# Optimization experiments

Measured on AMD Instinct MI355X. Metric: run time of the kernel, lower is better.

Reference implementation:

```python
import jax, jax.numpy as jnp
import numpy as np

N_NODES = 50000
N_EDGES = 1200000
D_FEAT = 64
HIDDEN = 32


def setup_inputs() -> dict:
    key = jax.random.key(0)
    ks = jax.random.split(key, 9)
    x = jax.random.normal(ks[0], (N_NODES, D_FEAT), dtype=jnp.float32)
    edge_index = jax.random.randint(ks[1], (2, N_EDGES), 0, N_NODES, dtype=jnp.int64)
    u = jax.random.normal(ks[2], (N_NODES,), dtype=jnp.float32)
    d_in = 2 * D_FEAT
    # MLP: Linear(d_in,H) -> relu -> Linear(H,H) -> relu -> Linear(H,1)
    W1 = jax.random.normal(ks[3], (d_in, HIDDEN), dtype=jnp.float32) / np.sqrt(d_in)
    b1 = jnp.zeros((HIDDEN,), dtype=jnp.float32)
    W2 = jax.random.normal(ks[4], (HIDDEN, HIDDEN), dtype=jnp.float32) / np.sqrt(HIDDEN)
    b2 = jnp.zeros((HIDDEN,), dtype=jnp.float32)
    W3 = jax.random.normal(ks[5], (HIDDEN, 1), dtype=jnp.float32) / np.sqrt(HIDDEN)
    b3 = jnp.zeros((1,), dtype=jnp.float32)
    return {"x": x, "edge_index": edge_index, "u": u,
            "W1": W1, "b1": b1, "W2": W2, "b2": b2, "W3": W3, "b3": b3}


def reference(x, edge_index, u, W1, b1, W2, b2, W3, b3):
    row, col = edge_index[0], edge_index[1]
    # gather + concat: [E, 2*D]
    x_edge = jnp.concatenate([x[row], x[col]], axis=-1)
    # per-edge MLP -> scalar weight per edge
    h = jax.nn.relu(x_edge @ W1 + b1)
    h = jax.nn.relu(h @ W2 + b2)
    edge_weight = (h @ W3 + b3)[:, 0]  # [E]
    # spmm: f[i] = sum_{e: row[e]==i} w_e * u[col[e]]
    f = jax.ops.segment_sum(edge_weight * u[col], row, num_segments=x.shape[0])
    return f
```

## Files before the change

### kernel.cpp

```cpp
#include <hip/hip_runtime.h>
#include <hip/hip_bf16.h>

#define N_NODES 50000
#define N_EDGES 1200000
#define N_TILES (N_NODES / 16)
#define W1T_STRIDE 72
#define K1_BLOCKS 782

#define N_BUCKETS 196
#define BUCKET_CAP 7168
#define EDGES_PER_BLOCK 1920
#define KA_BLOCKS 625
#define D1_BLOCKS (K1_BLOCKS + KA_BLOCKS)
#define KB_SPLIT 4

typedef __attribute__((ext_vector_type(8))) short short8;
typedef __attribute__((ext_vector_type(4))) float floatx4;

__device__ __forceinline__ unsigned short f32_to_bf16(float f) {
    unsigned int v = __float_as_uint(f);
    unsigned int r = v + 0x7FFFu + ((v >> 16) & 1u);
    return (unsigned short)(r >> 16);
}
__device__ __forceinline__ float bf16_to_f32(unsigned short s) {
    return __uint_as_float(((unsigned int)s) << 16);
}
__device__ __forceinline__ unsigned int pk_bf16x2_rn(float lo, float hi) {
    union { __hip_bfloat162 h; unsigned int u; } cv;
    cv.h = __float22bfloat162_rn(make_float2(lo, hi));
    return cv.u;
}
#define DPP_ROR_F32(x, N) \
    __int_as_float(__builtin_amdgcn_update_dpp( \
        0, __float_as_int(x), 0x120 + (N), 0xF, 0xF, false))

__global__ __launch_bounds__(256) void fused_pre_bin(
    const float* __restrict__ x, const float* __restrict__ W1,
    const float* __restrict__ b1,
    const int* __restrict__ row, const int* __restrict__ col,
    unsigned short* __restrict__ P1, unsigned short* __restrict__ P2,
    unsigned int* __restrict__ buf, int* __restrict__ cursor,
    float* __restrict__ out)
{
    __shared__ union {
        unsigned short W1t[64 * W1T_STRIDE];
        struct {
            unsigned short rankv[EDGES_PER_BLOCK];
            int hist[N_BUCKETS];
            int base[N_BUCKETS];
        } bin;
    } sh;

    const int tid = threadIdx.x;
    const int bid = blockIdx.x;

    if (bid < K1_BLOCKS) {
        const int gtid = bid * 256 + tid;
        for (int i = gtid; i < N_NODES; i += K1_BLOCKS * 256)
            out[i] = 0.0f;

        for (int e = tid; e < 128 * 32; e += 256) {
            const int kp = e >> 5, jp = e & 31;
            sh.W1t[((kp < 64) ? jp : jp + 32) * W1T_STRIDE + (kp & 63)] =
                f32_to_bf16(W1[e]);
        }
        __syncthreads();

        const int lane = tid & 63;
        const int n = lane & 15;
        const int q = lane >> 4;

        const int tile = bid * 4 + (tid >> 6);
        if (tile >= N_TILES) return;

        short8 bw[4][2];
        #pragma unroll
        for (int G = 0; G < 4; ++G)
            #pragma unroll
            for (int h = 0; h < 2; ++h)
                bw[G][h] = *(const short8*)
                    &sh.W1t[(n + 16 * G) * W1T_STRIDE + h * 32 + q * 8];
        const float bias0 = b1[n], bias1 = b1[n + 16];

        const int node = tile * 16 + n;
        const float4* xp  = (const float4*)(x + (size_t)node * 64 + q * 8);
        const float4 xa = xp[0], xb = xp[1];
        const float4* xp2 = (const float4*)(x + (size_t)node * 64 + 32 + q * 8);
        const float4 xc = xp2[0], xd = xp2[1];

        union S8 { short8 s; unsigned int w[4]; } A0, A1;
        A0.w[0] = pk_bf16x2_rn(xa.x, xa.y);
        A0.w[1] = pk_bf16x2_rn(xa.z, xa.w);
        A0.w[2] = pk_bf16x2_rn(xb.x, xb.y);
        A0.w[3] = pk_bf16x2_rn(xb.z, xb.w);
        A1.w[0] = pk_bf16x2_rn(xc.x, xc.y);
        A1.w[1] = pk_bf16x2_rn(xc.z, xc.w);
        A1.w[2] = pk_bf16x2_rn(xd.x, xd.y);
        A1.w[3] = pk_bf16x2_rn(xd.z, xd.w);
        const short8 a0 = A0.s, a1 = A1.s;

        floatx4 acc[4];
        #pragma unroll
        for (int G = 0; G < 4; ++G) {
            const float bi = (G == 0) ? bias0 : (G == 1) ? bias1 : 0.0f;
            acc[G] = (floatx4){bi, bi, bi, bi};
            acc[G] = __builtin_amdgcn_mfma_f32_16x16x32_bf16(a0, bw[G][0], acc[G], 0, 0, 0);
            acc[G] = __builtin_amdgcn_mfma_f32_16x16x32_bf16(a1, bw[G][1], acc[G], 0, 0, 0);
        }
        unsigned int* P1d = (unsigned int*)P1;
        unsigned int* P2d = (unsigned int*)P2;
        #pragma unroll
        for (int r = 0; r < 4; ++r) {
            const int nr = tile * 16 + q * 4 + r;
            P1d[(size_t)nr * 16 + n] = pk_bf16x2_rn(acc[0][r], acc[1][r]);
            P2d[(size_t)nr * 16 + n] = pk_bf16x2_rn(acc[2][r], acc[3][r]);
        }
    } else {
        for (int b = tid; b < N_BUCKETS; b += 256) sh.bin.hist[b] = 0;
        __syncthreads();

        const int blockStart = (bid - K1_BLOCKS) * EDGES_PER_BLOCK;

        for (int i = tid; i < EDGES_PER_BLOCK; i += 256) {
            const int r = row[blockStart + i];
            sh.bin.rankv[i] = (unsigned short)atomicAdd(&sh.bin.hist[r >> 8], 1);
        }
        __syncthreads();

        for (int b = tid; b < N_BUCKETS; b += 256)
            sh.bin.base[b] = atomicAdd(&cursor[b], sh.bin.hist[b]);
        __syncthreads();

        for (int i = tid; i < EDGES_PER_BLOCK; i += 256) {
            const int r = row[blockStart + i];
            const int c = col[blockStart + i];
            const int bin = r >> 8;
            buf[(size_t)bin * BUCKET_CAP + sh.bin.base[bin] + (int)sh.bin.rankv[i]] =
                ((unsigned int)(r & 255) << 24) | (unsigned int)c;
        }
    }
}

__global__ __launch_bounds__(512) void bucket_mlp(
    const float* __restrict__ u,
    const float* __restrict__ W2, const float* __restrict__ b2,
    const float* __restrict__ W3, const float* __restrict__ b3,
    const unsigned short* __restrict__ P1, const unsigned short* __restrict__ P2,
    const unsigned int* __restrict__ buf, const int* __restrict__ cursor,
    float* __restrict__ out)
{
    __shared__ float accs[256];
    const int tid = threadIdx.x;
    if (tid < 256) accs[tid] = 0.0f;

    const int b = blockIdx.x >> 2;
    const int s = blockIdx.x & (KB_SPLIT - 1);

    const int lane = tid & 63;
    const int n = lane & 15;
    const int q = lane >> 4;
    const int wave = tid >> 6;

    short8 bf0, bf1;
    #pragma unroll
    for (int i = 0; i < 8; ++i) {
        const int F = q * 4 + (i >> 1) + 16 * (i & 1);
        bf0[i] = (short)f32_to_bf16(W2[F * 32 + n]);
        bf1[i] = (short)f32_to_bf16(W2[F * 32 + n + 16]);
    }
    const float w3n0 = W3[n], w3n1 = W3[n + 16];
    const float b2n0 = b2[n], b2n1 = b2[n + 16];
    const float bias3 = b3[0];

    __syncthreads();

    const int cnt = cursor[b];
    const unsigned int* bb = buf + (size_t)b * BUCKET_CAP;
    const unsigned short* P1b = P1 + (size_t)b * 256 * 32;
    const int nch = (cnt + 31) >> 5;

    #pragma unroll 1
    for (int ch = s * 8 + wave; ch < nch; ch += KB_SPLIT * 8) {
        const int base0 = ch * 32;

        int rl[2], cI[2];
        #pragma unroll
        for (int t = 0; t < 2; ++t) {
            int e = base0 + t * 16 + n;
            if (e >= cnt) e = cnt - 1;
            const unsigned int ent = bb[e];
            rl[t] = (int)(ent >> 24);
            cI[t] = (int)(ent & 0x1FFFFu);
        }
        int r2 = 0; float u2 = 0.0f;
        if (n < 8) {
            const int eloc = base0 + 16 * (n >> 2) + 4 * q + (n & 3);
            const unsigned int ent2 = bb[(eloc < cnt) ? eloc : 0];
            r2 = (int)(ent2 >> 24);
            u2 = (eloc < cnt) ? u[ent2 & 0x1FFFFu] : 0.0f;
        }
        short8 v1[2], v2[2];
        #pragma unroll
        for (int t = 0; t < 2; ++t) {
            v1[t] = *(const short8*)(P1b + (size_t)rl[t] * 32 + q * 8);
            v2[t] = *(const short8*)(P2 + (size_t)cI[t] * 32 + q * 8);
        }

        float tr[2][4];
        #pragma unroll
        for (int t = 0; t < 2; ++t) {
            union VU { short8 s; unsigned int w[4]; };
            VU x1, x2, ar;
            x1.s = v1[t]; x2.s = v2[t];
            #pragma unroll
            for (int i = 0; i < 4; ++i) {
                const unsigned int w1 = x1.w[i], w2 = x2.w[i];
                float lo = __uint_as_float(w1 << 16) + __uint_as_float(w2 << 16);
                float hi = __uint_as_float(w1 & 0xFFFF0000u)
                         + __uint_as_float(w2 & 0xFFFF0000u);
                lo = fmaxf(lo, 0.0f);
                hi = fmaxf(hi, 0.0f);
                ar.w[i] = pk_bf16x2_rn(lo, hi);
            }
            const short8 a = ar.s;
            floatx4 d0 = {b2n0, b2n0, b2n0, b2n0};
            floatx4 d1 = {b2n1, b2n1, b2n1, b2n1};
            d0 = __builtin_amdgcn_mfma_f32_16x16x32_bf16(a, bf0, d0, 0, 0, 0);
            d1 = __builtin_amdgcn_mfma_f32_16x16x32_bf16(a, bf1, d1, 0, 0, 0);
            #pragma unroll
            for (int r = 0; r < 4; ++r)
                tr[t][r] = fmaxf(d0[r], 0.0f) * w3n0 + fmaxf(d1[r], 0.0f) * w3n1;
        }

        #pragma unroll
        for (int t = 0; t < 2; ++t)
            #pragma unroll
            for (int r = 0; r < 4; ++r) {
                float v = tr[t][r];
                v += DPP_ROR_F32(v, 1);
                v += DPP_ROR_F32(v, 2);
                v += DPP_ROR_F32(v, 4);
                v += DPP_ROR_F32(v, 8);
                tr[t][r] = v;
            }

        if (n < 8) {
            const float va0 = (n & 4) ? tr[1][0] : tr[0][0];
            const float va1 = (n & 4) ? tr[1][1] : tr[0][1];
            const float va2 = (n & 4) ? tr[1][2] : tr[0][2];
            const float va3 = (n & 4) ? tr[1][3] : tr[0][3];
            const float vb0 = (n & 2) ? va2 : va0;
            const float vb1 = (n & 2) ? va3 : va1;
            const float v   = (n & 1) ? vb1 : vb0;
            atomicAdd(&accs[r2], (v + bias3) * u2);
        }
    }

    __syncthreads();

    if (tid < 256) {
        const int node = b * 256 + tid;
        if (node < N_NODES) atomicAdd(out + node, accs[tid]);
    }
}

extern "C" void kernel_launch(void* const* d_in, const int* in_sizes, int n_in,
                              void* d_out, int out_size, void* d_ws, size_t ws_size,
                              hipStream_t stream)
{
    const float* x    = (const float*)d_in[0];
    const int*   eidx = (const int*)  d_in[1];
    const float* u    = (const float*)d_in[2];
    const float* W1   = (const float*)d_in[3];
    const float* b1   = (const float*)d_in[4];
    const float* W2   = (const float*)d_in[5];
    const float* b2   = (const float*)d_in[6];
    const float* W3   = (const float*)d_in[7];
    const float* b3   = (const float*)d_in[8];

    const int* row = eidx;
    const int* col = eidx + N_EDGES;

    unsigned short* P1 = (unsigned short*)d_ws;
    unsigned short* P2 = (unsigned short*)((char*)d_ws + (size_t)N_NODES * 64);
    unsigned int*  buf = (unsigned int*)((char*)d_ws + (size_t)N_NODES * 128);
    int* cursor = (int*)((char*)d_ws + (size_t)N_NODES * 128
                         + (size_t)N_BUCKETS * BUCKET_CAP * 4);
    float* out = (float*)d_out;

    hipMemsetAsync(cursor, 0, N_BUCKETS * sizeof(int), stream);

    fused_pre_bin<<<D1_BLOCKS, 256, 0, stream>>>(
        x, W1, b1, row, col, P1, P2, buf, cursor, out);

    bucket_mlp<<<N_BUCKETS * KB_SPLIT, 512, 0, stream>>>(
        u, W2, b2, W3, b3, P1, P2, buf, cursor, out);
}
```

Before: 132.1 us.

## Merge memset, prebin and bucket MLP into one cooperative persistent kernel

Replaces the memset plus two kernel launches with a single cooperative kernel that uses grid-wide syncs between zeroing, the binning/first-layer GEMM phase, and the per-bucket MLP/scatter phase. Work is distributed as persistent tasks over a grid sized from occupancy, and the bucket phase now uses 256-thread blocks with 8 splits per bucket instead of 512-thread blocks with 4. The aim is to remove launch gaps and the memset, at the cost of grid.sync overhead and a different occupancy/work balance. The old path is kept as a fallback when the cooperative launch fails.

```diff
diff --git a/kernel.cpp b/kernel.cpp
--- a/kernel.cpp
+++ b/kernel.cpp
@@ -1,18 +1,27 @@
 #include <hip/hip_runtime.h>
 #include <hip/hip_bf16.h>
+#include <hip/hip_cooperative_groups.h>
+
+namespace cg = cooperative_groups;
 
 #define N_NODES 50000
 #define N_EDGES 1200000
 #define N_TILES (N_NODES / 16)
-#define W1T_STRIDE 72
-#define K1_BLOCKS 782
 
 #define N_BUCKETS 196
 #define BUCKET_CAP 7168
 #define EDGES_PER_BLOCK 1920
 #define KA_BLOCKS 625
+#define GEMM_BLOCKS 782
+#define A1_TASKS (KA_BLOCKS + GEMM_BLOCKS)
+#define KB_SPLIT8 8
+#define KB_TASKS (N_BUCKETS * KB_SPLIT8)
+#define MAX_COOP_GRID 2048
+
+#define W1T_STRIDE_FB 72
+#define K1_BLOCKS 782
 #define D1_BLOCKS (K1_BLOCKS + KA_BLOCKS)
-#define KB_SPLIT 4
+#define KB_SPLIT_FB 4
 
 typedef __attribute__((ext_vector_type(8))) short short8;
 typedef __attribute__((ext_vector_type(4))) float floatx4;
@@ -33,6 +42,237 @@
 #define DPP_ROR_F32(x, N) \
     __int_as_float(__builtin_amdgcn_update_dpp( \
         0, __float_as_int(x), 0x120 + (N), 0xF, 0xF, false))
+
+__global__ __launch_bounds__(256, 8) void edgemlp_coop(
+    const float* __restrict__ x, const float* __restrict__ W1,
+    const float* __restrict__ b1,
+    const int* __restrict__ row, const int* __restrict__ col,
+    const float* __restrict__ u,
+    const float* __restrict__ W2, const float* __restrict__ b2,
+    const float* __restrict__ W3, const float* __restrict__ b3,
+    unsigned short* __restrict__ P1, unsigned short* __restrict__ P2,
+    unsigned int* __restrict__ buf, int* __restrict__ cursor,
+    float* __restrict__ out)
+{
+    __shared__ union {
+        unsigned short W1t[64 * 64];
+        struct {
+            unsigned short rankv[EDGES_PER_BLOCK];
+            int hist[N_BUCKETS];
+            int base[N_BUCKETS];
+        } bin;
+        float accs[256];
+    } sh;
+
+    cg::grid_group grid = cg::this_grid();
+
+    const int tid = threadIdx.x;
+    const int bid = blockIdx.x;
+    const int gstride = (int)gridDim.x;
+    const int gtid = bid * 256 + tid;
+
+    const int lane = tid & 63;
+    const int n = lane & 15;
+    const int q = lane >> 4;
+    const int wave = tid >> 6;
+
+    for (int i = gtid; i < N_NODES; i += gstride * 256) out[i] = 0.0f;
+    if (gtid < N_BUCKETS) cursor[gtid] = 0;
+
+    grid.sync();
+
+    for (int task = bid; task < A1_TASKS; task += gstride) {
+        if (task < KA_BLOCKS) {
+            for (int b = tid; b < N_BUCKETS; b += 256) sh.bin.hist[b] = 0;
+            __syncthreads();
+
+            const int blockStart = task * EDGES_PER_BLOCK;
+
+            for (int i = tid; i < EDGES_PER_BLOCK; i += 256) {
+                const int r = row[blockStart + i];
+                sh.bin.rankv[i] =
+                    (unsigned short)atomicAdd(&sh.bin.hist[r >> 8], 1);
+            }
+            __syncthreads();
+
+            for (int b = tid; b < N_BUCKETS; b += 256)
+                sh.bin.base[b] = atomicAdd(&cursor[b], sh.bin.hist[b]);
+            __syncthreads();
+
+            for (int i = tid; i < EDGES_PER_BLOCK; i += 256) {
+                const int r = row[blockStart + i];
+                const int c = col[blockStart + i];
+                const int bin = r >> 8;
+                buf[(size_t)bin * BUCKET_CAP + sh.bin.base[bin]
+                    + (int)sh.bin.rankv[i]] =
+                    ((unsigned int)(r & 255) << 24) | (unsigned int)c;
+            }
+        } else {
+            for (int e = tid; e < 128 * 32; e += 256) {
+                const int kp = e >> 5, jp = e & 31;
+                sh.W1t[((kp < 64) ? jp : jp + 32) * 64 + (kp & 63)] =
+                    f32_to_bf16(W1[e]);
+            }
+            __syncthreads();
+
+            const int tile = (task - KA_BLOCKS) * 4 + wave;
+            if (tile < N_TILES) {
+                short8 bw[4][2];
+                #pragma unroll
+                for (int G = 0; G < 4; ++G)
+                    #pragma unroll
+                    for (int h = 0; h < 2; ++h)
+                        bw[G][h] = *(const short8*)
+                            &sh.W1t[(n + 16 * G) * 64 + h * 32 + q * 8];
+                const float bias0 = b1[n], bias1 = b1[n + 16];
+
+                const int node = tile * 16 + n;
+                const float4* xp  = (const float4*)(x + (size_t)node * 64 + q * 8);
+                const float4 xa = xp[0], xb = xp[1];
+                const float4* xp2 = (const float4*)(x + (size_t)node * 64 + 32 + q * 8);
+                const float4 xc = xp2[0], xd = xp2[1];
+
+                union S8 { short8 s; unsigned int w[4]; } A0v, A1v;
+                A0v.w[0] = pk_bf16x2_rn(xa.x, xa.y);
+                A0v.w[1] = pk_bf16x2_rn(xa.z, xa.w);
+                A0v.w[2] = pk_bf16x2_rn(xb.x, xb.y);
+                A0v.w[3] = pk_bf16x2_rn(xb.z, xb.w);
+                A1v.w[0] = pk_bf16x2_rn(xc.x, xc.y);
+                A1v.w[1] = pk_bf16x2_rn(xc.z, xc.w);
+                A1v.w[2] = pk_bf16x2_rn(xd.x, xd.y);
+                A1v.w[3] = pk_bf16x2_rn(xd.z, xd.w);
+                const short8 a0 = A0v.s, a1 = A1v.s;
+
+                floatx4 acc[4];
+                #pragma unroll
+                for (int G = 0; G < 4; ++G) {
+                    const float bi = (G == 0) ? bias0 : (G == 1) ? bias1 : 0.0f;
+                    acc[G] = (floatx4){bi, bi, bi, bi};
+                    acc[G] = __builtin_amdgcn_mfma_f32_16x16x32_bf16(a0, bw[G][0], acc[G], 0, 0, 0);
+                    acc[G] = __builtin_amdgcn_mfma_f32_16x16x32_bf16(a1, bw[G][1], acc[G], 0, 0, 0);
+                }
+                unsigned int* P1d = (unsigned int*)P1;
+                unsigned int* P2d = (unsigned int*)P2;
+                #pragma unroll
+                for (int r = 0; r < 4; ++r) {
+                    const int nr = tile * 16 + q * 4 + r;
+                    P1d[(size_t)nr * 16 + n] = pk_bf16x2_rn(acc[0][r], acc[1][r]);
+                    P2d[(size_t)nr * 16 + n] = pk_bf16x2_rn(acc[2][r], acc[3][r]);
+                }
+            }
+        }
+        __syncthreads();
+    }
+
+    grid.sync();
+
+    short8 bf0, bf1;
+    #pragma unroll
+    for (int i = 0; i < 8; ++i) {
+        const int F = q * 4 + (i >> 1) + 16 * (i & 1);
+        bf0[i] = (short)f32_to_bf16(W2[F * 32 + n]);
+        bf1[i] = (short)f32_to_bf16(W2[F * 32 + n + 16]);
+    }
+    const float w3n0 = W3[n], w3n1 = W3[n + 16];
+    const float b2n0 = b2[n], b2n1 = b2[n + 16];
+    const float bias3 = b3[0];
+
+    for (int task = bid; task < KB_TASKS; task += gstride) {
+        const int b = task >> 3;
+        const int s = task & (KB_SPLIT8 - 1);
+
+        sh.accs[tid] = 0.0f;
+        __syncthreads();
+
+        const int cnt = cursor[b];
+        const unsigned int* bb = buf + (size_t)b * BUCKET_CAP;
+        const unsigned short* P1b = P1 + (size_t)b * 256 * 32;
+        const int nch = (cnt + 31) >> 5;
+
+        #pragma unroll 1
+        for (int ch = s * 4 + wave; ch < nch; ch += 32) {
+            const int base0 = ch * 32;
+
+            int rl[2], cI[2];
+            #pragma unroll
+            for (int t = 0; t < 2; ++t) {
+                int e = base0 + t * 16 + n;
+                if (e >= cnt) e = cnt - 1;
+                const unsigned int ent = bb[e];
+                rl[t] = (int)(ent >> 24);
+                cI[t] = (int)(ent & 0x1FFFFu);
+            }
+            int r2 = 0; float u2 = 0.0f;
+            if (n < 8) {
+                const int eloc = base0 + 16 * (n >> 2) + 4 * q + (n & 3);
+                const unsigned int ent2 = bb[(eloc < cnt) ? eloc : 0];
+                r2 = (int)(ent2 >> 24);
+                u2 = (eloc < cnt) ? u[ent2 & 0x1FFFFu] : 0.0f;
+            }
+            short8 v1[2], v2[2];
+            #pragma unroll
+            for (int t = 0; t < 2; ++t) {
+                v1[t] = *(const short8*)(P1b + (size_t)rl[t] * 32 + q * 8);
+                v2[t] = *(const short8*)(P2 + (size_t)cI[t] * 32 + q * 8);
+            }
+
+            float tr[2][4];
+            #pragma unroll
+            for (int t = 0; t < 2; ++t) {
+                union VU { short8 s; unsigned int w[4]; };
+                VU x1, x2, ar;
+                x1.s = v1[t]; x2.s = v2[t];
+                #pragma unroll
+                for (int i = 0; i < 4; ++i) {
+                    const unsigned int w1 = x1.w[i], w2 = x2.w[i];
+                    float lo = __uint_as_float(w1 << 16) + __uint_as_float(w2 << 16);
+                    float hi = __uint_as_float(w1 & 0xFFFF0000u)
+                             + __uint_as_float(w2 & 0xFFFF0000u);
+                    lo = fmaxf(lo, 0.0f);
+                    hi = fmaxf(hi, 0.0f);
+                    ar.w[i] = pk_bf16x2_rn(lo, hi);
+                }
+                const short8 a = ar.s;
+                floatx4 d0 = {b2n0, b2n0, b2n0, b2n0};
+                floatx4 d1 = {b2n1, b2n1, b2n1, b2n1};
+                d0 = __builtin_amdgcn_mfma_f32_16x16x32_bf16(a, bf0, d0, 0, 0, 0);
+                d1 = __builtin_amdgcn_mfma_f32_16x16x32_bf16(a, bf1, d1, 0, 0, 0);
+                #pragma unroll
+                for (int r = 0; r < 4; ++r)
+                    tr[t][r] = fmaxf(d0[r], 0.0f) * w3n0 + fmaxf(d1[r], 0.0f) * w3n1;
+            }
+
+            #pragma unroll
+            for (int t = 0; t < 2; ++t)
+                #pragma unroll
+                for (int r = 0; r < 4; ++r) {
+                    float v = tr[t][r];
+                    v += DPP_ROR_F32(v, 1);
+                    v += DPP_ROR_F32(v, 2);
+                    v += DPP_ROR_F32(v, 4);
+                    v += DPP_ROR_F32(v, 8);
+                    tr[t][r] = v;
+                }
+
+            if (n < 8) {
+                const float va0 = (n & 4) ? tr[1][0] : tr[0][0];
+                const float va1 = (n & 4) ? tr[1][1] : tr[0][1];
+                const float va2 = (n & 4) ? tr[1][2] : tr[0][2];
+                const float va3 = (n & 4) ? tr[1][3] : tr[0][3];
+                const float vb0 = (n & 2) ? va2 : va0;
+                const float vb1 = (n & 2) ? va3 : va1;
+                const float v   = (n & 1) ? vb1 : vb0;
+                atomicAdd(&sh.accs[r2], (v + bias3) * u2);
+            }
+        }
+
+        __syncthreads();
+
+        const int node = b * 256 + tid;
+        if (node < N_NODES) atomicAdd(out + node, sh.accs[tid]);
+        __syncthreads();
+    }
+}
 
 __global__ __launch_bounds__(256) void fused_pre_bin(
     const float* __restrict__ x, const float* __restrict__ W1,
@@ -43,7 +283,7 @@
     float* __restrict__ out)
 {
     __shared__ union {
-        unsigned short W1t[64 * W1T_STRIDE];
+        unsigned short W1t[64 * W1T_STRIDE_FB];
         struct {
             unsigned short rankv[EDGES_PER_BLOCK];
             int hist[N_BUCKETS];
@@ -61,7 +301,7 @@
 
         for (int e = tid; e < 128 * 32; e += 256) {
             const int kp = e >> 5, jp = e & 31;
-            sh.W1t[((kp < 64) ? jp : jp + 32) * W1T_STRIDE + (kp & 63)] =
+            sh.W1t[((kp < 64) ? jp : jp + 32) * W1T_STRIDE_FB + (kp & 63)] =
                 f32_to_bf16(W1[e]);
         }
         __syncthreads();
@@ -79,7 +319,7 @@
             #pragma unroll
             for (int h = 0; h < 2; ++h)
                 bw[G][h] = *(const short8*)
-                    &sh.W1t[(n + 16 * G) * W1T_STRIDE + h * 32 + q * 8];
+                    &sh.W1t[(n + 16 * G) * W1T_STRIDE_FB + h * 32 + q * 8];
         const float bias0 = b1[n], bias1 = b1[n + 16];
 
         const int node = tile * 16 + n;
@@ -154,7 +394,7 @@
     if (tid < 256) accs[tid] = 0.0f;
 
     const int b = blockIdx.x >> 2;
-    const int s = blockIdx.x & (KB_SPLIT - 1);
+    const int s = blockIdx.x & (KB_SPLIT_FB - 1);
 
     const int lane = tid & 63;
     const int n = lane & 15;
@@ -180,7 +420,7 @@
     const int nch = (cnt + 31) >> 5;
 
     #pragma unroll 1
-    for (int ch = s * 8 + wave; ch < nch; ch += KB_SPLIT * 8) {
+    for (int ch = s * 8 + wave; ch < nch; ch += KB_SPLIT_FB * 8) {
         const int base0 = ch * 32;
 
         int rl[2], cI[2];
@@ -288,11 +528,30 @@
                          + (size_t)N_BUCKETS * BUCKET_CAP * 4);
     float* out = (float*)d_out;
 
-    hipMemsetAsync(cursor, 0, N_BUCKETS * sizeof(int), stream);
-
-    fused_pre_bin<<<D1_BLOCKS, 256, 0, stream>>>(
-        x, W1, b1, row, col, P1, P2, buf, cursor, out);
-
-    bucket_mlp<<<N_BUCKETS * KB_SPLIT, 512, 0, stream>>>(
-        u, W2, b2, W3, b3, P1, P2, buf, cursor, out);
-}
+    int maxbpc = 0;
+    hipError_t qerr = hipOccupancyMaxActiveBlocksPerMultiprocessor(
+        &maxbpc, (const void*)edgemlp_coop, 256, 0);
+    int grid = (qerr == hipSuccess && maxbpc > 0) ? maxbpc * 256 : 0;
+    if (grid > MAX_COOP_GRID) grid = MAX_COOP_GRID;
+
+    bool done = false;
+    if (grid >= 512) {
+        void* args[] = {
+            (void*)&x, (void*)&W1, (void*)&b1, (void*)&row, (void*)&col,
+            (void*)&u, (void*)&W2, (void*)&b2, (void*)&W3, (void*)&b3,
+            (void*)&P1, (void*)&P2, (void*)&buf, (void*)&cursor, (void*)&out
+        };
+        hipError_t err = hipLaunchCooperativeKernel(
+            (const void*)edgemlp_coop, dim3(grid), dim3(256), args, 0, stream);
+        done = (err == hipSuccess);
+        if (!done) (void)hipGetLastError();
+    }
+
+    if (!done) {
+        hipMemsetAsync(cursor, 0, N_BUCKETS * sizeof(int), stream);
+        fused_pre_bin<<<D1_BLOCKS, 256, 0, stream>>>(
+            x, W1, b1, row, col, P1, P2, buf, cursor, out);
+        bucket_mlp<<<N_BUCKETS * KB_SPLIT_FB, 512, 0, stream>>>(
+            u, W2, b2, W3, b3, P1, P2, buf, cursor, out);
+    }
+}
```

New measurement: 351.2 us. +166.0%, slower.
